# Kernel optimization log

Measured on AMD Instinct MI355X. Metric: run time of the kernel, lower is better.

The kernel has to match this reference:

```python
import jax, jax.numpy as jnp
import numpy as np

HEAD_NUM = 4
EMB = 128
N_NODES = 50000
N_EDGES = 600000


def setup_inputs() -> dict:
    key = jax.random.key(0)
    k1, k2, k3, k4, k5, k6 = jax.random.split(key, 6)
    embeds = jax.random.normal(k1, (N_NODES, EMB), dtype=jnp.float32)
    qW = jax.random.normal(k2, (EMB, EMB), dtype=jnp.float32) * (1.0 / np.sqrt(EMB))
    kW = jax.random.normal(k3, (EMB, EMB), dtype=jnp.float32) * (1.0 / np.sqrt(EMB))
    vW = jax.random.normal(k4, (EMB, EMB), dtype=jnp.float32) * (1.0 / np.sqrt(EMB))
    rows = jax.random.randint(k5, (N_EDGES,), 0, N_NODES, dtype=jnp.int32)
    cols = jax.random.randint(k6, (N_EDGES,), 0, N_NODES, dtype=jnp.int32)
    return {"embeds": embeds, "qW": qW, "kW": kW, "vW": vW,
            "rows": rows, "cols": cols, "n_nodes": N_NODES}


def reference(embeds, qW, kW, vW, rows, cols, n_nodes):
    H = HEAD_NUM
    D = embeds.shape[1]
    Dh = D // H
    rowEmb = embeds[rows]                                   # [E, D] gather
    colEmb = embeds[cols]                                   # [E, D] gather
    q = (rowEmb @ qW).reshape(-1, H, Dh)                    # [E, H, Dh]
    k = (colEmb @ kW).reshape(-1, H, Dh)
    v = (colEmb @ vW).reshape(-1, H, Dh)
    att = jnp.einsum('ehd,ehd->eh', q, k)                   # per-edge per-head logits
    att = jnp.clip(att, -10.0, 10.0)
    expAtt = jnp.exp(att)                                   # [E, H]
    attNorm = jax.ops.segment_sum(expAtt, rows, num_segments=n_nodes)  # [N, H]
    att = expAtt / (attNorm[rows] + 1e-8)                   # segment softmax
    res = (att[..., None] * v).reshape(-1, D)               # [E, D]
    out = jax.ops.segment_sum(res, rows, num_segments=n_nodes)  # [N, D]
    return out
```

## Files before the change

kernel.cpp:

```cpp
#include <hip/hip_runtime.h>
#include <math.h>

#define EMB 128
#define HEADS 4
#define OS 140
#define CAP 64
#define CLAMP_L2 14.4269504088896f

typedef __attribute__((ext_vector_type(8))) _Float16 f16x8;
typedef __attribute__((ext_vector_type(4))) _Float16 f16x4;
typedef __attribute__((ext_vector_type(2))) _Float16 f16x2;
typedef __attribute__((ext_vector_type(4))) float f32x4;

__global__ __launch_bounds__(256) void prep_w(
    const float* __restrict__ Wq, const float* __restrict__ Wk, const float* __restrict__ Wv,
    _Float16* __restrict__ Wfrag, int* __restrict__ deg, int N)
{
    int flat = blockIdx.x * 256 + threadIdx.x;
    if (flat < 3 * 16384) {
        int m    = flat >> 14;
        int rem  = flat & 16383;
        int ct   = rem >> 11;
        int s    = (rem >> 9) & 3;
        int lane = (rem >> 3) & 63;
        int j    = rem & 7;
        int k = s * 32 + (lane >> 4) * 8 + j;
        int n = ct * 16 + (lane & 15);
        const float* Ws[3] = { Wq, Wk, Wv };
        float val = Ws[m][k * 128 + n];
        if (m == 0) val *= 1.44269504088896f;
        Wfrag[flat] = (_Float16)val;
    }
    if (flat < N) deg[flat] = 0;
}

__global__ __launch_bounds__(256) void mega_kernel(
    const float* __restrict__ embeds,
    const _Float16* __restrict__ Wfrag,
    _Float16* __restrict__ Qh, _Float16* __restrict__ KV,
    const int* __restrict__ rows, const int* __restrict__ cols,
    int* __restrict__ deg, unsigned short* __restrict__ slots,
    int N, int E, int PB, int S)
{
    __shared__ __align__(16) _Float16 sBuf[64 * OS];

    const int bid = blockIdx.x;
    const bool isProj = ((bid % S) == 0) && ((bid / S) < PB);

    if (!isProj) {
        int fidx = bid - min((bid + S - 1) / S, PB);
        int e = fidx * 256 + threadIdx.x;
        if (e < E) {
            int r = rows[e];
            int pos = atomicAdd(&deg[r], 1);
            if (pos < CAP) slots[(size_t)r * CAP + pos] = (unsigned short)cols[e];
        }
        return;
    }

    const int n0 = (bid / S) * 64;
    const int t  = threadIdx.x;

    #pragma unroll
    for (int j = 0; j < 8; j++) {
        int flat = t + j * 256;
        int row  = flat >> 5;
        int c4   = flat & 31;
        int gn   = n0 + row;
        float4 v = (gn < N) ? reinterpret_cast<const float4*>(embeds)[(size_t)gn * 32 + c4]
                            : make_float4(0.f, 0.f, 0.f, 0.f);
        f16x4 u = { (_Float16)v.x, (_Float16)v.y, (_Float16)v.z, (_Float16)v.w };
        *reinterpret_cast<f16x4*>(&sBuf[row * OS + c4 * 4]) = u;
    }
    __syncthreads();

    const int w    = t >> 6;
    const int lane = t & 63;
    const int nlo  = lane & 15;
    const int quad = lane >> 4;

    f16x8 a[4][4];
    #pragma unroll
    for (int strip = 0; strip < 4; strip++)
        #pragma unroll
        for (int s = 0; s < 4; s++)
            a[strip][s] = *reinterpret_cast<const f16x8*>(
                &sBuf[(16 * strip + nlo) * OS + s * 32 + quad * 8]);
    __syncthreads();

    const int rbase = quad * 4;

    #pragma unroll
    for (int u = 0; u < 2; u++) {
        const int ct = w * 2 + u;
        f16x8 b[4];
        #pragma unroll
        for (int s = 0; s < 4; s++)
            b[s] = *reinterpret_cast<const f16x8*>(
                Wfrag + ((size_t)(ct * 4 + s) * 64 + lane) * 8);
        const int lcol = ct * 16 + nlo;
        #pragma unroll
        for (int strip = 0; strip < 4; strip++) {
            f32x4 acc = { 0.f, 0.f, 0.f, 0.f };
            #pragma unroll
            for (int s = 0; s < 4; s++)
                acc = __builtin_amdgcn_mfma_f32_16x16x32_f16(a[strip][s], b[s], acc, 0, 0, 0);
            const int row = 16 * strip + rbase;
            #pragma unroll
            for (int r = 0; r < 4; r++)
                sBuf[(row + r) * OS + lcol] = (_Float16)acc[r];
        }
    }
    __syncthreads();
    #pragma unroll
    for (int j = 0; j < 4; j++) {
        int flat = j * 2048 + t * 8;
        int row  = flat >> 7;
        int col  = flat & 127;
        int gn   = n0 + row;
        if (gn < N) {
            f16x8 v = *reinterpret_cast<const f16x8*>(&sBuf[row * OS + col]);
            *reinterpret_cast<f16x8*>(&Qh[(size_t)gn * EMB + col]) = v;
        }
    }

    #pragma unroll
    for (int h = 0; h < 2; h++) {
        __syncthreads();
        const int m    = 1 + (w & 1);
        const int voff = (m == 2) ? 4 : 0;
        #pragma unroll
        for (int u = 0; u < 2; u++) {
            const int ct = 4 * h + (w >> 1) + 2 * u;
            const int T  = m * 8 + ct;
            f16x8 b[4];
            #pragma unroll
            for (int s = 0; s < 4; s++)
                b[s] = *reinterpret_cast<const f16x8*>(
                    Wfrag + ((size_t)(T * 4 + s) * 64 + lane) * 8);
            const int colh = (ct - 4 * h) * 16 + nlo;
            const int lidx = 8 * (colh >> 2) + (colh & 3) + voff;
            #pragma unroll
            for (int strip = 0; strip < 4; strip++) {
                f32x4 acc = { 0.f, 0.f, 0.f, 0.f };
                #pragma unroll
                for (int s = 0; s < 4; s++)
                    acc = __builtin_amdgcn_mfma_f32_16x16x32_f16(a[strip][s], b[s], acc, 0, 0, 0);
                const int row = 16 * strip + rbase;
                #pragma unroll
                for (int r = 0; r < 4; r++)
                    sBuf[(row + r) * OS + lidx] = (_Float16)acc[r];
            }
        }
        __syncthreads();
        #pragma unroll
        for (int j = 0; j < 4; j++) {
            int flat = j * 2048 + t * 8;
            int row  = flat >> 7;
            int col  = flat & 127;
            int gn   = n0 + row;
            if (gn < N) {
                f16x8 v = *reinterpret_cast<const f16x8*>(&sBuf[row * OS + col]);
                *reinterpret_cast<f16x8*>(&KV[(size_t)gn * 256 + 128 * h + col]) = v;
            }
        }
    }
}

__global__ __launch_bounds__(256) void node_fused(
    const _Float16* __restrict__ Qh, const _Float16* __restrict__ KV,
    const int* __restrict__ deg, const unsigned short* __restrict__ slots,
    float* __restrict__ out, int N)
{
    int n = blockIdx.x * 8 + (threadIdx.x >> 5);
    if (n >= N) return;
    int lane = threadIdx.x & 31;

    f16x4 qh = *reinterpret_cast<const f16x4*>(Qh + (size_t)n * EMB + lane * 4);
    f16x2 q01 = { qh.x, qh.y };
    f16x2 q23 = { qh.z, qh.w };

    int cnt = deg[n];
    if (cnt > CAP) cnt = CAP;
    const unsigned short* sl = slots + (size_t)n * CAP;
    const char* KVb = (const char*)KV;
    const unsigned loff = (unsigned)lane * 16u;

    float4 acc = make_float4(0.f, 0.f, 0.f, 0.f);
    float norm = 0.f;
    int i = 0;

    for (; i + 4 <= cnt; i += 4) {
        uint2 s4 = *reinterpret_cast<const uint2*>(sl + i);
        unsigned o0 = ((s4.x & 0xffffu) << 9) + loff;
        unsigned o1 = ((s4.x >> 16)     << 9) + loff;
        unsigned o2 = ((s4.y & 0xffffu) << 9) + loff;
        unsigned o3 = ((s4.y >> 16)     << 9) + loff;
        f16x8 kv0 = *reinterpret_cast<const f16x8*>(KVb + o0);
        f16x8 kv1 = *reinterpret_cast<const f16x8*>(KVb + o1);
        f16x8 kv2 = *reinterpret_cast<const f16x8*>(KVb + o2);
        f16x8 kv3 = *reinterpret_cast<const f16x8*>(KVb + o3);

        f16x2 k0a = __builtin_shufflevector(kv0, kv0, 0, 1);
        f16x2 k0b = __builtin_shufflevector(kv0, kv0, 2, 3);
        f16x2 k1a = __builtin_shufflevector(kv1, kv1, 0, 1);
        f16x2 k1b = __builtin_shufflevector(kv1, kv1, 2, 3);
        f16x2 k2a = __builtin_shufflevector(kv2, kv2, 0, 1);
        f16x2 k2b = __builtin_shufflevector(kv2, kv2, 2, 3);
        f16x2 k3a = __builtin_shufflevector(kv3, kv3, 0, 1);
        f16x2 k3b = __builtin_shufflevector(kv3, kv3, 2, 3);

        float d0 = __builtin_amdgcn_fdot2(k0a, q01, __builtin_amdgcn_fdot2(k0b, q23, 0.f, false), false);
        float d1 = __builtin_amdgcn_fdot2(k1a, q01, __builtin_amdgcn_fdot2(k1b, q23, 0.f, false), false);
        float d2 = __builtin_amdgcn_fdot2(k2a, q01, __builtin_amdgcn_fdot2(k2b, q23, 0.f, false), false);
        float d3 = __builtin_amdgcn_fdot2(k3a, q01, __builtin_amdgcn_fdot2(k3b, q23, 0.f, false), false);

        d0 += __shfl_xor(d0, 1); d1 += __shfl_xor(d1, 1); d2 += __shfl_xor(d2, 1); d3 += __shfl_xor(d3, 1);
        d0 += __shfl_xor(d0, 2); d1 += __shfl_xor(d1, 2); d2 += __shfl_xor(d2, 2); d3 += __shfl_xor(d3, 2);
        d0 += __shfl_xor(d0, 4); d1 += __shfl_xor(d1, 4); d2 += __shfl_xor(d2, 4); d3 += __shfl_xor(d3, 4);

        float ea0 = exp2f(fminf(CLAMP_L2, fmaxf(-CLAMP_L2, d0)));
        float ea1 = exp2f(fminf(CLAMP_L2, fmaxf(-CLAMP_L2, d1)));
        float ea2 = exp2f(fminf(CLAMP_L2, fmaxf(-CLAMP_L2, d2)));
        float ea3 = exp2f(fminf(CLAMP_L2, fmaxf(-CLAMP_L2, d3)));

        acc.x = fmaf(ea0, (float)kv0[4], acc.x);
        acc.y = fmaf(ea0, (float)kv0[5], acc.y);
        acc.z = fmaf(ea0, (float)kv0[6], acc.z);
        acc.w = fmaf(ea0, (float)kv0[7], acc.w);
        acc.x = fmaf(ea1, (float)kv1[4], acc.x);
        acc.y = fmaf(ea1, (float)kv1[5], acc.y);
        acc.z = fmaf(ea1, (float)kv1[6], acc.z);
        acc.w = fmaf(ea1, (float)kv1[7], acc.w);
        acc.x = fmaf(ea2, (float)kv2[4], acc.x);
        acc.y = fmaf(ea2, (float)kv2[5], acc.y);
        acc.z = fmaf(ea2, (float)kv2[6], acc.z);
        acc.w = fmaf(ea2, (float)kv2[7], acc.w);
        acc.x = fmaf(ea3, (float)kv3[4], acc.x);
        acc.y = fmaf(ea3, (float)kv3[5], acc.y);
        acc.z = fmaf(ea3, (float)kv3[6], acc.z);
        acc.w = fmaf(ea3, (float)kv3[7], acc.w);
        norm += ea0 + ea1 + ea2 + ea3;
    }
    for (; i < cnt; i++) {
        unsigned o0 = ((unsigned)sl[i] << 9) + loff;
        f16x8 kv0 = *reinterpret_cast<const f16x8*>(KVb + o0);
        f16x2 k0a = __builtin_shufflevector(kv0, kv0, 0, 1);
        f16x2 k0b = __builtin_shufflevector(kv0, kv0, 2, 3);
        float d0 = __builtin_amdgcn_fdot2(k0a, q01, __builtin_amdgcn_fdot2(k0b, q23, 0.f, false), false);
        d0 += __shfl_xor(d0, 1);
        d0 += __shfl_xor(d0, 2);
        d0 += __shfl_xor(d0, 4);
        float ea0 = exp2f(fminf(CLAMP_L2, fmaxf(-CLAMP_L2, d0)));
        acc.x = fmaf(ea0, (float)kv0[4], acc.x);
        acc.y = fmaf(ea0, (float)kv0[5], acc.y);
        acc.z = fmaf(ea0, (float)kv0[6], acc.z);
        acc.w = fmaf(ea0, (float)kv0[7], acc.w);
        norm += ea0;
    }

    float inv = 1.f / (norm + 1e-8f);
    acc.x *= inv; acc.y *= inv; acc.z *= inv; acc.w *= inv;
    reinterpret_cast<float4*>(out + (size_t)n * EMB)[lane] = acc;
}

extern "C" void kernel_launch(void* const* d_in, const int* in_sizes, int n_in,
                              void* d_out, int out_size, void* d_ws, size_t ws_size,
                              hipStream_t stream) {
    const float* embeds = (const float*)d_in[0];
    const float* qW     = (const float*)d_in[1];
    const float* kW     = (const float*)d_in[2];
    const float* vW     = (const float*)d_in[3];
    const int*   rows   = (const int*)d_in[4];
    const int*   cols   = (const int*)d_in[5];

    const int N = in_sizes[0] / EMB;
    const int E = in_sizes[4];

    _Float16*       Qh    = (_Float16*)d_ws;
    _Float16*       KV    = Qh + (size_t)N * EMB;
    _Float16*       Wfrag = KV + (size_t)N * 256;
    int*            deg   = (int*)(Wfrag + 3 * 16384);
    unsigned short* slots = (unsigned short*)(deg + N);

    float* out = (float*)d_out;

    const int GB = ((N > 3 * 16384 ? N : 3 * 16384) + 255) / 256;
    prep_w<<<GB, 256, 0, stream>>>(qW, kW, vW, Wfrag, deg, N);

    const int PB = (N + 63) / 64;
    const int FB = (E + 255) / 256;
    const int S  = (PB + FB) / PB > 1 ? (PB + FB) / PB : 1;
    mega_kernel<<<PB + FB, 256, 0, stream>>>(embeds, Wfrag, Qh, KV,
                                             rows, cols, deg, slots, N, E, PB, S);

    node_fused<<<(N + 7) / 8, 256, 0, stream>>>(Qh, KV, deg, slots, out, N);
}
```

Measured before the change: 169.4 us.

## Split edge bucketing from projection kernel and unroll neighbor loop by eight

Moves the edge-slot fill (atomic degree counting) out of the interleaved projection mega-kernel and into the weight-prep kernel. The degree reset becomes a hipMemsetAsync, and the projection now runs as its own kernel. The neighbor aggregation loop in node_fused gains an 8-way unrolled path so more gathers are in flight per iteration. This trades the old overlap of atomics with projection compute for simpler kernels, and adds one extra memset launch plus higher register pressure from the wider unroll.

```diff
diff --git a/kernel.cpp b/kernel.cpp
--- a/kernel.cpp
+++ b/kernel.cpp
@@ -12,11 +12,24 @@
 typedef __attribute__((ext_vector_type(2))) _Float16 f16x2;
 typedef __attribute__((ext_vector_type(4))) float f32x4;
 
-__global__ __launch_bounds__(256) void prep_w(
+__global__ __launch_bounds__(256) void prep_fill(
     const float* __restrict__ Wq, const float* __restrict__ Wk, const float* __restrict__ Wv,
-    _Float16* __restrict__ Wfrag, int* __restrict__ deg, int N)
+    _Float16* __restrict__ Wfrag,
+    const int* __restrict__ rows, const int* __restrict__ cols,
+    int* __restrict__ deg, unsigned short* __restrict__ slots,
+    int E, int FB)
 {
-    int flat = blockIdx.x * 256 + threadIdx.x;
+    const int bid = blockIdx.x;
+    if (bid < FB) {
+        int e = bid * 256 + threadIdx.x;
+        if (e < E) {
+            int r = rows[e];
+            int pos = atomicAdd(&deg[r], 1);
+            if (pos < CAP) slots[(size_t)r * CAP + pos] = (unsigned short)cols[e];
+        }
+        return;
+    }
+    int flat = (bid - FB) * 256 + threadIdx.x;
     if (flat < 3 * 16384) {
         int m    = flat >> 14;
         int rem  = flat & 16383;
@@ -31,34 +44,17 @@
         if (m == 0) val *= 1.44269504088896f;
         Wfrag[flat] = (_Float16)val;
     }
-    if (flat < N) deg[flat] = 0;
 }
 
-__global__ __launch_bounds__(256) void mega_kernel(
+__global__ __launch_bounds__(256) void proj_kernel(
     const float* __restrict__ embeds,
     const _Float16* __restrict__ Wfrag,
     _Float16* __restrict__ Qh, _Float16* __restrict__ KV,
-    const int* __restrict__ rows, const int* __restrict__ cols,
-    int* __restrict__ deg, unsigned short* __restrict__ slots,
-    int N, int E, int PB, int S)
+    int N)
 {
     __shared__ __align__(16) _Float16 sBuf[64 * OS];
 
-    const int bid = blockIdx.x;
-    const bool isProj = ((bid % S) == 0) && ((bid / S) < PB);
-
-    if (!isProj) {
-        int fidx = bid - min((bid + S - 1) / S, PB);
-        int e = fidx * 256 + threadIdx.x;
-        if (e < E) {
-            int r = rows[e];
-            int pos = atomicAdd(&deg[r], 1);
-            if (pos < CAP) slots[(size_t)r * CAP + pos] = (unsigned short)cols[e];
-        }
-        return;
-    }
-
-    const int n0 = (bid / S) * 64;
+    const int n0 = blockIdx.x * 64;
     const int t  = threadIdx.x;
 
     #pragma unroll
@@ -190,64 +186,92 @@
     float norm = 0.f;
     int i = 0;
 
+    for (; i + 8 <= cnt; i += 8) {
+        uint4 s8 = *reinterpret_cast<const uint4*>(sl + i);
+        unsigned off0 = ((s8.x & 0xffffu) << 9) + loff;
+        unsigned off1 = ((s8.x >> 16)     << 9) + loff;
+        unsigned off2 = ((s8.y & 0xffffu) << 9) + loff;
+        unsigned off3 = ((s8.y >> 16)     << 9) + loff;
+        unsigned off4 = ((s8.z & 0xffffu) << 9) + loff;
+        unsigned off5 = ((s8.z >> 16)     << 9) + loff;
+        unsigned off6 = ((s8.w & 0xffffu) << 9) + loff;
+        unsigned off7 = ((s8.w >> 16)     << 9) + loff;
+        f16x8 kv[8];
+        kv[0] = *reinterpret_cast<const f16x8*>(KVb + off0);
+        kv[1] = *reinterpret_cast<const f16x8*>(KVb + off1);
+        kv[2] = *reinterpret_cast<const f16x8*>(KVb + off2);
+        kv[3] = *reinterpret_cast<const f16x8*>(KVb + off3);
+        kv[4] = *reinterpret_cast<const f16x8*>(KVb + off4);
+        kv[5] = *reinterpret_cast<const f16x8*>(KVb + off5);
+        kv[6] = *reinterpret_cast<const f16x8*>(KVb + off6);
+        kv[7] = *reinterpret_cast<const f16x8*>(KVb + off7);
+
+        float d[8];
+        #pragma unroll
+        for (int u = 0; u < 8; u++) {
+            f16x2 ka = __builtin_shufflevector(kv[u], kv[u], 0, 1);
+            f16x2 kb = __builtin_shufflevector(kv[u], kv[u], 2, 3);
+            d[u] = __builtin_amdgcn_fdot2(ka, q01,
+                       __builtin_amdgcn_fdot2(kb, q23, 0.f, false), false);
+        }
+        #pragma unroll
+        for (int u = 0; u < 8; u++) {
+            d[u] += __shfl_xor(d[u], 1);
+            d[u] += __shfl_xor(d[u], 2);
+            d[u] += __shfl_xor(d[u], 4);
+        }
+        #pragma unroll
+        for (int u = 0; u < 8; u++) {
+            float ea = exp2f(fminf(CLAMP_L2, fmaxf(-CLAMP_L2, d[u])));
+            acc.x = fmaf(ea, (float)kv[u][4], acc.x);
+            acc.y = fmaf(ea, (float)kv[u][5], acc.y);
+            acc.z = fmaf(ea, (float)kv[u][6], acc.z);
+            acc.w = fmaf(ea, (float)kv[u][7], acc.w);
+            norm += ea;
+        }
+    }
     for (; i + 4 <= cnt; i += 4) {
         uint2 s4 = *reinterpret_cast<const uint2*>(sl + i);
-        unsigned o0 = ((s4.x & 0xffffu) << 9) + loff;
-        unsigned o1 = ((s4.x >> 16)     << 9) + loff;
-        unsigned o2 = ((s4.y & 0xffffu) << 9) + loff;
-        unsigned o3 = ((s4.y >> 16)     << 9) + loff;
-        f16x8 kv0 = *reinterpret_cast<const f16x8*>(KVb + o0);
-        f16x8 kv1 = *reinterpret_cast<const f16x8*>(KVb + o1);
-        f16x8 kv2 = *reinterpret_cast<const f16x8*>(KVb + o2);
-        f16x8 kv3 = *reinterpret_cast<const f16x8*>(KVb + o3);
-
-        f16x2 k0a = __builtin_shufflevector(kv0, kv0, 0, 1);
-        f16x2 k0b = __builtin_shufflevector(kv0, kv0, 2, 3);
-        f16x2 k1a = __builtin_shufflevector(kv1, kv1, 0, 1);
-        f16x2 k1b = __builtin_shufflevector(kv1, kv1, 2, 3);
-        f16x2 k2a = __builtin_shufflevector(kv2, kv2, 0, 1);
-        f16x2 k2b = __builtin_shufflevector(kv2, kv2, 2, 3);
-        f16x2 k3a = __builtin_shufflevector(kv3, kv3, 0, 1);
-        f16x2 k3b = __builtin_shufflevector(kv3, kv3, 2, 3);
-
-        float d0 = __builtin_amdgcn_fdot2(k0a, q01, __builtin_amdgcn_fdot2(k0b, q23, 0.f, false), false);
-        float d1 = __builtin_amdgcn_fdot2(k1a, q01, __builtin_amdgcn_fdot2(k1b, q23, 0.f, false), false);
-        float d2 = __builtin_amdgcn_fdot2(k2a, q01, __builtin_amdgcn_fdot2(k2b, q23, 0.f, false), false);
-        float d3 = __builtin_amdgcn_fdot2(k3a, q01, __builtin_amdgcn_fdot2(k3b, q23, 0.f, false), false);
-
-        d0 += __shfl_xor(d0, 1); d1 += __shfl_xor(d1, 1); d2 += __shfl_xor(d2, 1); d3 += __shfl_xor(d3, 1);
-        d0 += __shfl_xor(d0, 2); d1 += __shfl_xor(d1, 2); d2 += __shfl_xor(d2, 2); d3 += __shfl_xor(d3, 2);
-        d0 += __shfl_xor(d0, 4); d1 += __shfl_xor(d1, 4); d2 += __shfl_xor(d2, 4); d3 += __shfl_xor(d3, 4);
-
-        float ea0 = exp2f(fminf(CLAMP_L2, fmaxf(-CLAMP_L2, d0)));
-        float ea1 = exp2f(fminf(CLAMP_L2, fmaxf(-CLAMP_L2, d1)));
-        float ea2 = exp2f(fminf(CLAMP_L2, fmaxf(-CLAMP_L2, d2)));
-        float ea3 = exp2f(fminf(CLAMP_L2, fmaxf(-CLAMP_L2, d3)));
-
-        acc.x = fmaf(ea0, (float)kv0[4], acc.x);
-        acc.y = fmaf(ea0, (float)kv0[5], acc.y);
-        acc.z = fmaf(ea0, (float)kv0[6], acc.z);
-        acc.w = fmaf(ea0, (float)kv0[7], acc.w);
-        acc.x = fmaf(ea1, (float)kv1[4], acc.x);
-        acc.y = fmaf(ea1, (float)kv1[5], acc.y);
-        acc.z = fmaf(ea1, (float)kv1[6], acc.z);
-        acc.w = fmaf(ea1, (float)kv1[7], acc.w);
-        acc.x = fmaf(ea2, (float)kv2[4], acc.x);
-        acc.y = fmaf(ea2, (float)kv2[5], acc.y);
-        acc.z = fmaf(ea2, (float)kv2[6], acc.z);
-        acc.w = fmaf(ea2, (float)kv2[7], acc.w);
-        acc.x = fmaf(ea3, (float)kv3[4], acc.x);
-        acc.y = fmaf(ea3, (float)kv3[5], acc.y);
-        acc.z = fmaf(ea3, (float)kv3[6], acc.z);
-        acc.w = fmaf(ea3, (float)kv3[7], acc.w);
-        norm += ea0 + ea1 + ea2 + ea3;
+        unsigned off0 = ((s4.x & 0xffffu) << 9) + loff;
+        unsigned off1 = ((s4.x >> 16)     << 9) + loff;
+        unsigned off2 = ((s4.y & 0xffffu) << 9) + loff;
+        unsigned off3 = ((s4.y >> 16)     << 9) + loff;
+        f16x8 kv[4];
+        kv[0] = *reinterpret_cast<const f16x8*>(KVb + off0);
+        kv[1] = *reinterpret_cast<const f16x8*>(KVb + off1);
+        kv[2] = *reinterpret_cast<const f16x8*>(KVb + off2);
+        kv[3] = *reinterpret_cast<const f16x8*>(KVb + off3);
+        float d[4];
+        #pragma unroll
+        for (int u = 0; u < 4; u++) {
+            f16x2 ka = __builtin_shufflevector(kv[u], kv[u], 0, 1);
+            f16x2 kb = __builtin_shufflevector(kv[u], kv[u], 2, 3);
+            d[u] = __builtin_amdgcn_fdot2(ka, q01,
+                       __builtin_amdgcn_fdot2(kb, q23, 0.f, false), false);
+        }
+        #pragma unroll
+        for (int u = 0; u < 4; u++) {
+            d[u] += __shfl_xor(d[u], 1);
+            d[u] += __shfl_xor(d[u], 2);
+            d[u] += __shfl_xor(d[u], 4);
+        }
+        #pragma unroll
+        for (int u = 0; u < 4; u++) {
+            float ea = exp2f(fminf(CLAMP_L2, fmaxf(-CLAMP_L2, d[u])));
+            acc.x = fmaf(ea, (float)kv[u][4], acc.x);
+            acc.y = fmaf(ea, (float)kv[u][5], acc.y);
+            acc.z = fmaf(ea, (float)kv[u][6], acc.z);
+            acc.w = fmaf(ea, (float)kv[u][7], acc.w);
+            norm += ea;
+        }
     }
     for (; i < cnt; i++) {
         unsigned o0 = ((unsigned)sl[i] << 9) + loff;
         f16x8 kv0 = *reinterpret_cast<const f16x8*>(KVb + o0);
         f16x2 k0a = __builtin_shufflevector(kv0, kv0, 0, 1);
         f16x2 k0b = __builtin_shufflevector(kv0, kv0, 2, 3);
-        float d0 = __builtin_amdgcn_fdot2(k0a, q01, __builtin_amdgcn_fdot2(k0b, q23, 0.f, false), false);
+        float d0 = __builtin_amdgcn_fdot2(k0a, q01,
+                       __builtin_amdgcn_fdot2(k0b, q23, 0.f, false), false);
         d0 += __shfl_xor(d0, 1);
         d0 += __shfl_xor(d0, 2);
         d0 += __shfl_xor(d0, 4);
@@ -285,14 +309,15 @@
 
     float* out = (float*)d_out;
 
-    const int GB = ((N > 3 * 16384 ? N : 3 * 16384) + 255) / 256;
-    prep_w<<<GB, 256, 0, stream>>>(qW, kW, vW, Wfrag, deg, N);
+    (void)hipMemsetAsync(deg, 0, (size_t)N * sizeof(int), stream);
+
+    const int FB = (E + 255) / 256;
+    const int WB = (3 * 16384 + 255) / 256;
+    prep_fill<<<FB + WB, 256, 0, stream>>>(qW, kW, vW, Wfrag,
+                                           rows, cols, deg, slots, E, FB);
 
     const int PB = (N + 63) / 64;
-    const int FB = (E + 255) / 256;
-    const int S  = (PB + FB) / PB > 1 ? (PB + FB) / PB : 1;
-    mega_kernel<<<PB + FB, 256, 0, stream>>>(embeds, Wfrag, Qh, KV,
-                                             rows, cols, deg, slots, N, E, PB, S);
+    proj_kernel<<<PB, 256, 0, stream>>>(embeds, Wfrag, Qh, KV, N);
 
     node_fused<<<(N + 7) / 8, 256, 0, stream>>>(Qh, KV, deg, slots, out, N);
 }
```

Measured after the change: 181.5 us. 7.2% more time.

## Make projection blocks persistent over two tiles with register prefetch of next tile

Applied to the files above, without the earlier changes.

Halves the number of projection blocks so each one loops over two 64-node tiles. Embedding rows for the next tile are loaded into registers while the MFMA work for the current tile runs, to hide global load latency. The cost is fewer projection blocks in flight, so less parallelism, plus extra register pressure from the 8 prefetched float4 values. The interleaving of projection blocks with the fill blocks is recomputed for the new block count.

```diff
diff --git a/kernel.cpp b/kernel.cpp
--- a/kernel.cpp
+++ b/kernel.cpp
@@ -40,15 +40,15 @@
     _Float16* __restrict__ Qh, _Float16* __restrict__ KV,
     const int* __restrict__ rows, const int* __restrict__ cols,
     int* __restrict__ deg, unsigned short* __restrict__ slots,
-    int N, int E, int PB, int S)
+    int N, int E, int PB, int PBP, int S)
 {
     __shared__ __align__(16) _Float16 sBuf[64 * OS];
 
     const int bid = blockIdx.x;
-    const bool isProj = ((bid % S) == 0) && ((bid / S) < PB);
+    const bool isProj = ((bid % S) == 0) && ((bid / S) < PBP);
 
     if (!isProj) {
-        int fidx = bid - min((bid + S - 1) / S, PB);
+        int fidx = bid - min((bid + S - 1) / S, PBP);
         int e = fidx * 256 + threadIdx.x;
         if (e < E) {
             int r = rows[e];
@@ -58,88 +58,75 @@
         return;
     }
 
-    const int n0 = (bid / S) * 64;
-    const int t  = threadIdx.x;
-
-    #pragma unroll
-    for (int j = 0; j < 8; j++) {
-        int flat = t + j * 256;
-        int row  = flat >> 5;
-        int c4   = flat & 31;
-        int gn   = n0 + row;
-        float4 v = (gn < N) ? reinterpret_cast<const float4*>(embeds)[(size_t)gn * 32 + c4]
-                            : make_float4(0.f, 0.f, 0.f, 0.f);
-        f16x4 u = { (_Float16)v.x, (_Float16)v.y, (_Float16)v.z, (_Float16)v.w };
-        *reinterpret_cast<f16x4*>(&sBuf[row * OS + c4 * 4]) = u;
-    }
-    __syncthreads();
-
+    const int t    = threadIdx.x;
     const int w    = t >> 6;
     const int lane = t & 63;
     const int nlo  = lane & 15;
     const int quad = lane >> 4;
-
-    f16x8 a[4][4];
-    #pragma unroll
-    for (int strip = 0; strip < 4; strip++)
-        #pragma unroll
-        for (int s = 0; s < 4; s++)
-            a[strip][s] = *reinterpret_cast<const f16x8*>(
-                &sBuf[(16 * strip + nlo) * OS + s * 32 + quad * 8]);
-    __syncthreads();
-
     const int rbase = quad * 4;
 
-    #pragma unroll
-    for (int u = 0; u < 2; u++) {
-        const int ct = w * 2 + u;
-        f16x8 b[4];
-        #pragma unroll
-        for (int s = 0; s < 4; s++)
-            b[s] = *reinterpret_cast<const f16x8*>(
-                Wfrag + ((size_t)(ct * 4 + s) * 64 + lane) * 8);
-        const int lcol = ct * 16 + nlo;
-        #pragma unroll
-        for (int strip = 0; strip < 4; strip++) {
-            f32x4 acc = { 0.f, 0.f, 0.f, 0.f };
+    const int srow = t >> 5;
+    float4 r[8];
+
+    int tile = bid / S;
+    {
+        #pragma unroll
+        for (int j = 0; j < 8; j++) {
+            int flat = t + j * 256;
+            int row  = flat >> 5;
+            int c4   = flat & 31;
+            int gn   = tile * 64 + row;
+            r[j] = (gn < N) ? reinterpret_cast<const float4*>(embeds)[(size_t)gn * 32 + c4]
+                            : make_float4(0.f, 0.f, 0.f, 0.f);
+        }
+    }
+
+    for (; tile < PB; tile += PBP) {
+        const int n0   = tile * 64;
+        const int next = tile + PBP;
+
+        __syncthreads();
+
+        #pragma unroll
+        for (int j = 0; j < 8; j++) {
+            int flat = t + j * 256;
+            int row  = flat >> 5;
+            int c4   = flat & 31;
+            f16x4 u = { (_Float16)r[j].x, (_Float16)r[j].y, (_Float16)r[j].z, (_Float16)r[j].w };
+            *reinterpret_cast<f16x4*>(&sBuf[row * OS + c4 * 4]) = u;
+        }
+        __syncthreads();
+
+        f16x8 a[4][4];
+        #pragma unroll
+        for (int strip = 0; strip < 4; strip++)
             #pragma unroll
             for (int s = 0; s < 4; s++)
-                acc = __builtin_amdgcn_mfma_f32_16x16x32_f16(a[strip][s], b[s], acc, 0, 0, 0);
-            const int row = 16 * strip + rbase;
-            #pragma unroll
-            for (int r = 0; r < 4; r++)
-                sBuf[(row + r) * OS + lcol] = (_Float16)acc[r];
-        }
-    }
-    __syncthreads();
-    #pragma unroll
-    for (int j = 0; j < 4; j++) {
-        int flat = j * 2048 + t * 8;
-        int row  = flat >> 7;
-        int col  = flat & 127;
-        int gn   = n0 + row;
-        if (gn < N) {
-            f16x8 v = *reinterpret_cast<const f16x8*>(&sBuf[row * OS + col]);
-            *reinterpret_cast<f16x8*>(&Qh[(size_t)gn * EMB + col]) = v;
-        }
-    }
-
-    #pragma unroll
-    for (int h = 0; h < 2; h++) {
+                a[strip][s] = *reinterpret_cast<const f16x8*>(
+                    &sBuf[(16 * strip + nlo) * OS + s * 32 + quad * 8]);
         __syncthreads();
-        const int m    = 1 + (w & 1);
-        const int voff = (m == 2) ? 4 : 0;
+
+        if (next < PB) {
+            #pragma unroll
+            for (int j = 0; j < 8; j++) {
+                int flat = t + j * 256;
+                int row  = flat >> 5;
+                int c4   = flat & 31;
+                int gn   = next * 64 + row;
+                r[j] = (gn < N) ? reinterpret_cast<const float4*>(embeds)[(size_t)gn * 32 + c4]
+                                : make_float4(0.f, 0.f, 0.f, 0.f);
+            }
+        }
+
         #pragma unroll
         for (int u = 0; u < 2; u++) {
-            const int ct = 4 * h + (w >> 1) + 2 * u;
-            const int T  = m * 8 + ct;
+            const int ct = w * 2 + u;
             f16x8 b[4];
             #pragma unroll
             for (int s = 0; s < 4; s++)
                 b[s] = *reinterpret_cast<const f16x8*>(
-                    Wfrag + ((size_t)(T * 4 + s) * 64 + lane) * 8);
-            const int colh = (ct - 4 * h) * 16 + nlo;
-            const int lidx = 8 * (colh >> 2) + (colh & 3) + voff;
+                    Wfrag + ((size_t)(ct * 4 + s) * 64 + lane) * 8);
+            const int lcol = ct * 16 + nlo;
             #pragma unroll
             for (int strip = 0; strip < 4; strip++) {
                 f32x4 acc = { 0.f, 0.f, 0.f, 0.f };
@@ -148,8 +135,8 @@
                     acc = __builtin_amdgcn_mfma_f32_16x16x32_f16(a[strip][s], b[s], acc, 0, 0, 0);
                 const int row = 16 * strip + rbase;
                 #pragma unroll
-                for (int r = 0; r < 4; r++)
-                    sBuf[(row + r) * OS + lidx] = (_Float16)acc[r];
+                for (int rr = 0; rr < 4; rr++)
+                    sBuf[(row + rr) * OS + lcol] = (_Float16)acc[rr];
             }
         }
         __syncthreads();
@@ -161,7 +148,49 @@
             int gn   = n0 + row;
             if (gn < N) {
                 f16x8 v = *reinterpret_cast<const f16x8*>(&sBuf[row * OS + col]);
-                *reinterpret_cast<f16x8*>(&KV[(size_t)gn * 256 + 128 * h + col]) = v;
+                *reinterpret_cast<f16x8*>(&Qh[(size_t)gn * EMB + col]) = v;
+            }
+        }
+
+        #pragma unroll
+        for (int h = 0; h < 2; h++) {
+            __syncthreads();
+            const int m    = 1 + (w & 1);
+            const int voff = (m == 2) ? 4 : 0;
+            #pragma unroll
+            for (int u = 0; u < 2; u++) {
+                const int ct = 4 * h + (w >> 1) + 2 * u;
+                const int T  = m * 8 + ct;
+                f16x8 b[4];
+                #pragma unroll
+                for (int s = 0; s < 4; s++)
+                    b[s] = *reinterpret_cast<const f16x8*>(
+                        Wfrag + ((size_t)(T * 4 + s) * 64 + lane) * 8);
+                const int colh = (ct - 4 * h) * 16 + nlo;
+                const int lidx = 8 * (colh >> 2) + (colh & 3) + voff;
+                #pragma unroll
+                for (int strip = 0; strip < 4; strip++) {
+                    f32x4 acc = { 0.f, 0.f, 0.f, 0.f };
+                    #pragma unroll
+                    for (int s = 0; s < 4; s++)
+                        acc = __builtin_amdgcn_mfma_f32_16x16x32_f16(a[strip][s], b[s], acc, 0, 0, 0);
+                    const int row = 16 * strip + rbase;
+                    #pragma unroll
+                    for (int rr = 0; rr < 4; rr++)
+                        sBuf[(row + rr) * OS + lidx] = (_Float16)acc[rr];
+                }
+            }
+            __syncthreads();
+            #pragma unroll
+            for (int j = 0; j < 4; j++) {
+                int flat = j * 2048 + t * 8;
+                int row  = flat >> 7;
+                int col  = flat & 127;
+                int gn   = n0 + row;
+                if (gn < N) {
+                    f16x8 v = *reinterpret_cast<const f16x8*>(&sBuf[row * OS + col]);
+                    *reinterpret_cast<f16x8*>(&KV[(size_t)gn * 256 + 128 * h + col]) = v;
+                }
             }
         }
     }
@@ -288,11 +317,12 @@
     const int GB = ((N > 3 * 16384 ? N : 3 * 16384) + 255) / 256;
     prep_w<<<GB, 256, 0, stream>>>(qW, kW, vW, Wfrag, deg, N);
 
-    const int PB = (N + 63) / 64;
-    const int FB = (E + 255) / 256;
-    const int S  = (PB + FB) / PB > 1 ? (PB + FB) / PB : 1;
-    mega_kernel<<<PB + FB, 256, 0, stream>>>(embeds, Wfrag, Qh, KV,
-                                             rows, cols, deg, slots, N, E, PB, S);
+    const int PB  = (N + 63) / 64;
+    const int PBP = (PB + 1) / 2;
+    const int FB  = (E + 255) / 256;
+    int S = (PBP + FB) / PBP; if (S < 1) S = 1;
+    mega_kernel<<<PBP + FB, 256, 0, stream>>>(embeds, Wfrag, Qh, KV,
+                                              rows, cols, deg, slots, N, E, PB, PBP, S);
 
     node_fused<<<(N + 7) / 8, 256, 0, stream>>>(Qh, KV, deg, slots, out, N);
 }
```

Result: no change. 171.5 us (+1.3%).

## Fuse three launches into one cooperative persistent kernel with grid syncs

Applied to the files above, without the earlier changes.

Replaces the separate weight-prep, projection/bucketing and per-node attention launches with one cooperative kernel. It runs a persistent grid capped at 1024 blocks and uses grid.sync between phases, with half the blocks on projection tiles and half on edge bucketing. The aim is to remove launch gaps and kernel boundaries. In exchange, the grid is smaller, so each block loops over many tiles, and the two grid-wide barriers add cost. The old three-kernel path is kept as a fallback.

```diff
diff --git a/kernel.cpp b/kernel.cpp
--- a/kernel.cpp
+++ b/kernel.cpp
@@ -1,4 +1,5 @@
 #include <hip/hip_runtime.h>
+#include <hip/hip_cooperative_groups.h>
 #include <math.h>
 
 #define EMB 128
@@ -6,61 +7,45 @@
 #define OS 140
 #define CAP 64
 #define CLAMP_L2 14.4269504088896f
+#define NUM_CU 256
+
+namespace cg = cooperative_groups;
 
 typedef __attribute__((ext_vector_type(8))) _Float16 f16x8;
 typedef __attribute__((ext_vector_type(4))) _Float16 f16x4;
 typedef __attribute__((ext_vector_type(2))) _Float16 f16x2;
 typedef __attribute__((ext_vector_type(4))) float f32x4;
 
-__global__ __launch_bounds__(256) void prep_w(
-    const float* __restrict__ Wq, const float* __restrict__ Wk, const float* __restrict__ Wv,
-    _Float16* __restrict__ Wfrag, int* __restrict__ deg, int N)
-{
-    int flat = blockIdx.x * 256 + threadIdx.x;
-    if (flat < 3 * 16384) {
-        int m    = flat >> 14;
-        int rem  = flat & 16383;
-        int ct   = rem >> 11;
-        int s    = (rem >> 9) & 3;
-        int lane = (rem >> 3) & 63;
-        int j    = rem & 7;
-        int k = s * 32 + (lane >> 4) * 8 + j;
-        int n = ct * 16 + (lane & 15);
-        const float* Ws[3] = { Wq, Wk, Wv };
-        float val = Ws[m][k * 128 + n];
-        if (m == 0) val *= 1.44269504088896f;
-        Wfrag[flat] = (_Float16)val;
-    }
-    if (flat < N) deg[flat] = 0;
-}
-
-__global__ __launch_bounds__(256) void mega_kernel(
-    const float* __restrict__ embeds,
-    const _Float16* __restrict__ Wfrag,
-    _Float16* __restrict__ Qh, _Float16* __restrict__ KV,
-    const int* __restrict__ rows, const int* __restrict__ cols,
-    int* __restrict__ deg, unsigned short* __restrict__ slots,
-    int N, int E, int PB, int S)
-{
-    __shared__ __align__(16) _Float16 sBuf[64 * OS];
-
-    const int bid = blockIdx.x;
-    const bool isProj = ((bid % S) == 0) && ((bid / S) < PB);
-
-    if (!isProj) {
-        int fidx = bid - min((bid + S - 1) / S, PB);
-        int e = fidx * 256 + threadIdx.x;
-        if (e < E) {
-            int r = rows[e];
-            int pos = atomicAdd(&deg[r], 1);
-            if (pos < CAP) slots[(size_t)r * CAP + pos] = (unsigned short)cols[e];
-        }
-        return;
-    }
-
-    const int n0 = (bid / S) * 64;
-    const int t  = threadIdx.x;
-
+
+__device__ __forceinline__ void w_prep_elem(
+    int flat, const float* Wq, const float* Wk, const float* Wv, _Float16* Wfrag)
+{
+    int m    = flat >> 14;
+    int rem  = flat & 16383;
+    int ct   = rem >> 11;
+    int s    = (rem >> 9) & 3;
+    int lane = (rem >> 3) & 63;
+    int j    = rem & 7;
+    int k = s * 32 + (lane >> 4) * 8 + j;
+    int n = ct * 16 + (lane & 15);
+    const float* Ws[3] = { Wq, Wk, Wv };
+    float val = Ws[m][k * 128 + n];
+    if (m == 0) val *= 1.44269504088896f;
+    Wfrag[flat] = (_Float16)val;
+}
+
+__device__ __forceinline__ void proj_tile(
+    _Float16* sBuf, int n0, int t,
+    const float* __restrict__ embeds, const _Float16* __restrict__ Wfrag,
+    _Float16* __restrict__ Qh, _Float16* __restrict__ KV, int N)
+{
+    const int w    = t >> 6;
+    const int lane = t & 63;
+    const int nlo  = lane & 15;
+    const int quad = lane >> 4;
+    const int rbase = quad * 4;
+
+    __syncthreads();
     #pragma unroll
     for (int j = 0; j < 8; j++) {
         int flat = t + j * 256;
@@ -74,11 +59,6 @@
     }
     __syncthreads();
 
-    const int w    = t >> 6;
-    const int lane = t & 63;
-    const int nlo  = lane & 15;
-    const int quad = lane >> 4;
-
     f16x8 a[4][4];
     #pragma unroll
     for (int strip = 0; strip < 4; strip++)
@@ -87,8 +67,6 @@
             a[strip][s] = *reinterpret_cast<const f16x8*>(
                 &sBuf[(16 * strip + nlo) * OS + s * 32 + quad * 8]);
     __syncthreads();
-
-    const int rbase = quad * 4;
 
     #pragma unroll
     for (int u = 0; u < 2; u++) {
@@ -107,8 +85,8 @@
                 acc = __builtin_amdgcn_mfma_f32_16x16x32_f16(a[strip][s], b[s], acc, 0, 0, 0);
             const int row = 16 * strip + rbase;
             #pragma unroll
-            for (int r = 0; r < 4; r++)
-                sBuf[(row + r) * OS + lcol] = (_Float16)acc[r];
+            for (int rr = 0; rr < 4; rr++)
+                sBuf[(row + rr) * OS + lcol] = (_Float16)acc[rr];
         }
     }
     __syncthreads();
@@ -148,8 +126,8 @@
                     acc = __builtin_amdgcn_mfma_f32_16x16x32_f16(a[strip][s], b[s], acc, 0, 0, 0);
                 const int row = 16 * strip + rbase;
                 #pragma unroll
-                for (int r = 0; r < 4; r++)
-                    sBuf[(row + r) * OS + lidx] = (_Float16)acc[r];
+                for (int rr = 0; rr < 4; rr++)
+                    sBuf[(row + rr) * OS + lidx] = (_Float16)acc[rr];
             }
         }
         __syncthreads();
@@ -167,15 +145,12 @@
     }
 }
 
-__global__ __launch_bounds__(256) void node_fused(
+__device__ __forceinline__ void node_body(
+    int n, int lane,
     const _Float16* __restrict__ Qh, const _Float16* __restrict__ KV,
     const int* __restrict__ deg, const unsigned short* __restrict__ slots,
-    float* __restrict__ out, int N)
-{
-    int n = blockIdx.x * 8 + (threadIdx.x >> 5);
-    if (n >= N) return;
-    int lane = threadIdx.x & 31;
-
+    float* __restrict__ out)
+{
     f16x4 qh = *reinterpret_cast<const f16x4*>(Qh + (size_t)n * EMB + lane * 4);
     f16x2 q01 = { qh.x, qh.y };
     f16x2 q23 = { qh.z, qh.w };
@@ -264,6 +239,97 @@
     reinterpret_cast<float4*>(out + (size_t)n * EMB)[lane] = acc;
 }
 
+__global__ __launch_bounds__(256, 4) void fused_all(
+    const float* __restrict__ embeds,
+    const float* __restrict__ Wq, const float* __restrict__ Wk, const float* __restrict__ Wv,
+    const int* __restrict__ rows, const int* __restrict__ cols,
+    _Float16* __restrict__ Wfrag, _Float16* __restrict__ Qh, _Float16* __restrict__ KV,
+    int* __restrict__ deg, unsigned short* __restrict__ slots,
+    float* __restrict__ out, int N, int E, int PB, int PROJB, int G)
+{
+    __shared__ __align__(16) _Float16 sBuf[64 * OS];
+
+    cg::grid_group grid = cg::this_grid();
+    const int bid = blockIdx.x;
+    const int t   = threadIdx.x;
+
+    {
+        const int WLIM = 3 * 16384;
+        const int lim  = (N > WLIM) ? N : WLIM;
+        for (int flat = bid * 256 + t; flat < lim; flat += G * 256) {
+            if (flat < WLIM) w_prep_elem(flat, Wq, Wk, Wv, Wfrag);
+            if (flat < N)    deg[flat] = 0;
+        }
+    }
+    __threadfence();
+    grid.sync();
+
+    if (bid < PROJB) {
+        for (int tile = bid; tile < PB; tile += PROJB)
+            proj_tile(sBuf, tile * 64, t, embeds, Wfrag, Qh, KV, N);
+    } else {
+        const int stride = (G - PROJB) * 256;
+        for (int e = (bid - PROJB) * 256 + t; e < E; e += stride) {
+            int r = rows[e];
+            int pos = atomicAdd(&deg[r], 1);
+            if (pos < CAP) slots[(size_t)r * CAP + pos] = (unsigned short)cols[e];
+        }
+    }
+    __threadfence();
+    grid.sync();
+
+    {
+        const int NCH = (N + 7) / 8;
+        for (int c = bid; c < NCH; c += G) {
+            int n = c * 8 + (t >> 5);
+            if (n < N) node_body(n, t & 31, Qh, KV, deg, slots, out);
+        }
+    }
+}
+
+__global__ __launch_bounds__(256) void prep_w(
+    const float* __restrict__ Wq, const float* __restrict__ Wk, const float* __restrict__ Wv,
+    _Float16* __restrict__ Wfrag, int* __restrict__ deg, int N)
+{
+    int flat = blockIdx.x * 256 + threadIdx.x;
+    if (flat < 3 * 16384) w_prep_elem(flat, Wq, Wk, Wv, Wfrag);
+    if (flat < N) deg[flat] = 0;
+}
+
+__global__ __launch_bounds__(256) void mega_kernel(
+    const float* __restrict__ embeds,
+    const _Float16* __restrict__ Wfrag,
+    _Float16* __restrict__ Qh, _Float16* __restrict__ KV,
+    const int* __restrict__ rows, const int* __restrict__ cols,
+    int* __restrict__ deg, unsigned short* __restrict__ slots,
+    int N, int E, int PB, int S)
+{
+    __shared__ __align__(16) _Float16 sBuf[64 * OS];
+    const int bid = blockIdx.x;
+    const bool isProj = ((bid % S) == 0) && ((bid / S) < PB);
+    if (!isProj) {
+        int fidx = bid - min((bid + S - 1) / S, PB);
+        int e = fidx * 256 + threadIdx.x;
+        if (e < E) {
+            int r = rows[e];
+            int pos = atomicAdd(&deg[r], 1);
+            if (pos < CAP) slots[(size_t)r * CAP + pos] = (unsigned short)cols[e];
+        }
+        return;
+    }
+    proj_tile(sBuf, (bid / S) * 64, threadIdx.x, embeds, Wfrag, Qh, KV, N);
+}
+
+__global__ __launch_bounds__(256) void node_fused(
+    const _Float16* __restrict__ Qh, const _Float16* __restrict__ KV,
+    const int* __restrict__ deg, const unsigned short* __restrict__ slots,
+    float* __restrict__ out, int N)
+{
+    int n = blockIdx.x * 8 + (threadIdx.x >> 5);
+    if (n >= N) return;
+    node_body(n, threadIdx.x & 31, Qh, KV, deg, slots, out);
+}
+
 extern "C" void kernel_launch(void* const* d_in, const int* in_sizes, int n_in,
                               void* d_out, int out_size, void* d_ws, size_t ws_size,
                               hipStream_t stream) {
@@ -285,14 +351,41 @@
 
     float* out = (float*)d_out;
 
-    const int GB = ((N > 3 * 16384 ? N : 3 * 16384) + 255) / 256;
-    prep_w<<<GB, 256, 0, stream>>>(qW, kW, vW, Wfrag, deg, N);
-
     const int PB = (N + 63) / 64;
-    const int FB = (E + 255) / 256;
-    const int S  = (PB + FB) / PB > 1 ? (PB + FB) / PB : 1;
-    mega_kernel<<<PB + FB, 256, 0, stream>>>(embeds, Wfrag, Qh, KV,
-                                             rows, cols, deg, slots, N, E, PB, S);
-
-    node_fused<<<(N + 7) / 8, 256, 0, stream>>>(Qh, KV, deg, slots, out, N);
-}
+
+    static int coopG = -2;
+    if (coopG == -2) {
+        int b = 0;
+        hipError_t qe = hipOccupancyMaxActiveBlocksPerMultiprocessor(
+            &b, (const void*)fused_all, 256, 0);
+        coopG = (qe == hipSuccess && b > 0) ? b * NUM_CU : -1;
+        if (coopG > 1024) coopG = 1024;
+    }
+
+    bool launched = false;
+    if (coopG >= 256) {
+        int G = coopG, PROJB = G / 2;
+        int Ni = N, Ei = E, PBi = PB;
+        void* args[] = { (void*)&embeds, (void*)&qW, (void*)&kW, (void*)&vW,
+                         (void*)&rows, (void*)&cols,
+                         (void*)&Wfrag, (void*)&Qh, (void*)&KV,
+                         (void*)&deg, (void*)&slots, (void*)&out,
+                         (void*)&Ni, (void*)&Ei, (void*)&PBi, (void*)&PROJB, (void*)&G };
+        hipError_t err = hipLaunchCooperativeKernel((void*)fused_all, dim3(G), dim3(256),
+                                                    args, 0, stream);
+        launched = (err == hipSuccess);
+        if (!launched) coopG = -1;
+    }
+
+    if (!launched) {
+        const int GB = ((N > 3 * 16384 ? N : 3 * 16384) + 255) / 256;
+        prep_w<<<GB, 256, 0, stream>>>(qW, kW, vW, Wfrag, deg, N);
+
+        const int FB = (E + 255) / 256;
+        int S = (PB + FB) / PB; if (S < 1) S = 1;
+        mega_kernel<<<PB + FB, 256, 0, stream>>>(embeds, Wfrag, Qh, KV,
+                                                 rows, cols, deg, slots, N, E, PB, S);
+
+        node_fused<<<(N + 7) / 8, 256, 0, stream>>>(Qh, KV, deg, slots, out, N);
+    }
+}
```

New measurement: 404.0 us. 2.38x slower.
